# Performance work log

Hardware: AMD Instinct MI355X
Metric: run time of the kernel (lower is better)

Reference implementation:

```python
import jax, jax.numpy as jnp
import numpy as np
from math import sqrt

B, D, N, L, H, P = 32, 64, 254, 16, 128, 96  # batch, channels, patch_num, patch_len, hidden, pred_len


def positional_encoding(n, d):
    # standard sinusoidal PE, shape (n, d)
    pos = np.arange(n)[:, None].astype(np.float32)
    div = np.exp(np.arange(0, d, 2).astype(np.float32) * (-np.log(10000.0) / d))
    pe = np.zeros((n, d), dtype=np.float32)
    pe[:, 0::2] = np.sin(pos * div)
    pe[:, 1::2] = np.cos(pos * div)
    return jnp.asarray(pe)


def setup_inputs() -> dict:
    key = jax.random.key(0)
    ks = jax.random.split(key, 7)
    s = 0.05
    return {
        "x": jax.random.normal(ks[0], (B, D, N, L), dtype=jnp.float32),
        "W_enc": jax.random.normal(ks[1], (L, H), dtype=jnp.float32) * s,
        "b_enc": jax.random.normal(ks[2], (H,), dtype=jnp.float32) * s,
        "W1": jax.random.normal(ks[3], (L, H), dtype=jnp.float32) * s,
        "b1": jax.random.normal(ks[4], (H,), dtype=jnp.float32) * s,
        "W2": jax.random.normal(ks[5], (H, P), dtype=jnp.float32) * s,
        "b2": jax.random.normal(ks[6], (P,), dtype=jnp.float32) * s,
        "pos_embed": positional_encoding(N, H),  # buffer, not learned
    }


def reference(x, W_enc, b_enc, W1, b1, W2, b2, pos_embed):
    p = x  # detached clone in torch; same values
    # encode patches: (B,D,N,L) @ (L,H) -> (B,D,N,H), plus PE (N,H) broadcast
    c = jnp.einsum("bdnl,lh->bdnh", x, W_enc) + b_enc + pos_embed
    # score_i = sum_j c_i . c_j / sqrt(H)  ==  c_i . (sum_j c_j) / sqrt(H)
    csum = jnp.sum(c, axis=-2, keepdims=True)            # (B,D,1,H)
    score = jnp.sum(c * csum, axis=-1, keepdims=True) / sqrt(H)  # (B,D,N,1)
    weight = score / jnp.sum(jnp.abs(score), axis=-2, keepdims=True)
    pooled = jnp.sum(x * weight, axis=-2)                # (B,D,L)
    # FeedForward (dropout inactive at eval)
    h = jax.nn.leaky_relu(pooled @ W1 + b1, negative_slope=0.2)
    out = h @ W2 + b2                                    # (B,D,P)
    return out.transpose(0, 2, 1), p                     # (B,P,D), (B,D,N,L)
```

## Files before the change

### kernel.cpp

```cpp
#include <hip/hip_runtime.h>

#define B_ 32
#define D_ 64
#define N_ 254
#define L_ 16
#define H_ 128
#define P_ 96
#define PAIRS (B_*D_)
#define XPAIR (N_*L_)
#define OUT0  (B_*P_*D_)

#define WS_M    128
#define WS_VK   384
#define WS_BW   400
#define WS_BK   416
#define WS_G    432
#define WS_PK   4496
#define WS_KP   4752

typedef float f32x4 __attribute__((ext_vector_type(4)));

__global__ __launch_bounds__(256) void preK(const float* __restrict__ pos,
                                            float* __restrict__ ws) {
    __shared__ float red[256];
    int t = threadIdx.x;
    int h = t & 127, j = t >> 7;
    int n0 = blockIdx.x * 16;
    float acc = 0.f;
    #pragma unroll
    for (int r = 0; r < 8; r++) {
        int n = n0 + j + 2 * r;
        if (n < N_) acc += pos[n * H_ + h];
    }
    red[t] = acc;
    __syncthreads();
    if (t < 128) ws[WS_KP + blockIdx.x * 128 + t] = red[t] + red[t + 128];
}

__global__ __launch_bounds__(128) void pre2b(const float* __restrict__ W_enc,
                                             const float* __restrict__ b_enc,
                                             const float* __restrict__ pos,
                                             float* __restrict__ ws) {
    __shared__ float Ks[128], bL[128], pLDS[128], red[128], red2[128];
    __shared__ float WL[2048];
    int t = threadIdx.x;
    int n = blockIdx.x;

    {
        float b = b_enc[t];
        float s = 254.f * b;
        #pragma unroll
        for (int g = 0; g < 16; g++) s += ws[WS_KP + g * 128 + t];
        Ks[t] = s;
        bL[t] = b;
    }

    if (n < N_) {
        pLDS[t] = pos[n * H_ + t];
        __syncthreads();
        {
            int l = t >> 3, c = t & 7;
            const float* w = W_enc + l * H_ + c * 16;
            const float* p = pLDS + c * 16;
            float s = 0.f;
            #pragma unroll
            for (int i = 0; i < 16; i++) s += p[i] * w[i];
            red[t] = s;
            red2[t] = pLDS[t] * Ks[t];
        }
        __syncthreads();
        if (t < 16) {
            float s = 0.f;
            #pragma unroll
            for (int c = 0; c < 8; c++) s += red[t * 8 + c];
            ws[WS_G + n * 16 + t] = s;
        }
        if (t >= 64) {
            int lane = t - 64;
            float s = red2[lane] + red2[lane + 64];
            for (int off = 32; off; off >>= 1) s += __shfl_down(s, off);
            if (lane == 0) ws[WS_PK + n] = s;
        }
    } else {
        for (int i = t; i < 512; i += 128) {
            float4 v = ((const float4*)W_enc)[i];
            float* p = &WL[i * 4];
            p[0] = v.x; p[1] = v.y; p[2] = v.z; p[3] = v.w;
        }
        __syncthreads();
        #pragma unroll
        for (int e0 = 0; e0 < 2; e0++) {
            int e = e0 * 128 + t;
            int l1 = e >> 4, l2 = e & 15;
            float s = 0.f;
            for (int h = 0; h < H_; h++) s += WL[l1 * H_ + h] * WL[l2 * H_ + h];
            ws[WS_M + e] = s;
        }
        if (t < 16) {
            float s1 = 0.f, s2 = 0.f;
            for (int h = 0; h < H_; h++) {
                float w = WL[t * H_ + h];
                s1 += w * Ks[h];
                s2 += w * bL[h];
            }
            ws[WS_VK + t] = s1;
            ws[WS_BW + t] = s2;
        }
        if (t == 16) {
            float s = 0.f;
            for (int h = 0; h < H_; h++) s += bL[h] * Ks[h];
            ws[WS_BK] = s;
        }
    }
}

__global__ __launch_bounds__(256) void mainker(const float* __restrict__ x,
                                               const float* __restrict__ W1,
                                               const float* __restrict__ b1,
                                               const float* __restrict__ W2,
                                               const float* __restrict__ b2,
                                               const float* __restrict__ ws,
                                               float* __restrict__ out) {
    __shared__ float xf[N_ * 17 + 16];
    __shared__ float red[256];
    __shared__ float scoreS[N_];
    __shared__ float xsS[16], vS[16], pooledS[16], hS[128];
    __shared__ float s0S, denomS;

    int t  = threadIdx.x;
    int bd = blockIdx.x;

    const f32x4* xv = (const f32x4*)(x + (size_t)bd * XPAIR);
    f32x4*       cv = (f32x4*)(out + OUT0) + (size_t)bd * (XPAIR / 4);

    f32x4 v0 = xv[t];
    f32x4 v1 = xv[t + 256];
    f32x4 v2 = xv[t + 512];
    f32x4 v3 = {0.f, 0.f, 0.f, 0.f};
    bool has3 = (t < 248);
    if (has3) v3 = xv[t + 768];

    cv[t]       = v0;
    cv[t + 256] = v1;
    cv[t + 512] = v2;
    if (has3) cv[t + 768] = v3;

    #define UNPACK(vv, ii) { int idx = (ii) * 4; float* p = &xf[(idx >> 4) * 17 + (idx & 15)]; \
                             p[0] = vv[0]; p[1] = vv[1]; p[2] = vv[2]; p[3] = vv[3]; }
    UNPACK(v0, t); UNPACK(v1, t + 256); UNPACK(v2, t + 512);
    if (has3) UNPACK(v3, t + 768);
    #undef UNPACK
    __syncthreads();

    {
        int l = t & 15, g = t >> 4;
        float s = 0.f;
        for (int n = g; n < N_; n += 16) s += xf[n * 17 + l];
        red[t] = s;
    }
    __syncthreads();

    if (t < 16) {
        float xsv = 0.f;
        #pragma unroll
        for (int g = 0; g < 16; g++) xsv += red[g * 16 + t];
        xsS[t] = xsv;
        float s = ws[WS_VK + t];
        #pragma unroll
        for (int l2 = 0; l2 < 16; l2++) s += __shfl(xsv, l2) * ws[WS_M + l2 * 16 + t];
        vS[t] = s;
        float s0p = xsv * ws[WS_BW + t];
        #pragma unroll
        for (int off = 8; off; off >>= 1) s0p += __shfl_down(s0p, off);
        if (t == 0) s0S = ws[WS_BK] + s0p;
    }
    __syncthreads();

    if (t < N_) {
        const float* Gn = ws + WS_G + t * 16;
        float s = s0S + ws[WS_PK + t];
        #pragma unroll
        for (int l = 0; l < 16; l++) s += xf[t * 17 + l] * vS[l] + xsS[l] * Gn[l];
        scoreS[t] = s;
    }
    __syncthreads();

    if (t < 64) {
        float s = 0.f;
        for (int n = t; n < N_; n += 64) s += fabsf(scoreS[n]);
        for (int off = 32; off; off >>= 1) s += __shfl_down(s, off);
        if (t == 0) denomS = s;
    }
    {
        int l = t & 15, g = t >> 4;
        float s = 0.f;
        for (int n = g; n < N_; n += 16) s += xf[n * 17 + l] * scoreS[n];
        red[t] = s;
    }
    __syncthreads();
    if (t < 16) {
        float invd = 1.0f / denomS;
        float s = 0.f;
        #pragma unroll
        for (int g = 0; g < 16; g++) s += red[g * 16 + t];
        pooledS[t] = s * invd;
    }
    __syncthreads();

    if (t < 128) {
        float s = b1[t];
        #pragma unroll
        for (int l = 0; l < 16; l++) s += pooledS[l] * W1[l * H_ + t];
        hS[t] = s > 0.f ? s : 0.2f * s;
    }
    __syncthreads();

    if (t < 96) {
        float s = b2[t];
        for (int j = 0; j < 128; j++) s += hS[j] * W2[j * P_ + t];
        int b = bd >> 6, d = bd & 63;
        out[b * (P_ * D_) + t * D_ + d] = s;
    }
}

extern "C" void kernel_launch(void* const* d_in, const int* in_sizes, int n_in,
                              void* d_out, int out_size, void* d_ws, size_t ws_size,
                              hipStream_t stream) {
    const float* x     = (const float*)d_in[0];
    const float* W_enc = (const float*)d_in[1];
    const float* b_enc = (const float*)d_in[2];
    const float* W1    = (const float*)d_in[3];
    const float* b1    = (const float*)d_in[4];
    const float* W2    = (const float*)d_in[5];
    const float* b2    = (const float*)d_in[6];
    const float* pos   = (const float*)d_in[7];
    float* ws  = (float*)d_ws;
    float* out = (float*)d_out;

    hipLaunchKernelGGL(preK,   dim3(16),    dim3(256), 0, stream, pos, ws);
    hipLaunchKernelGGL(pre2b,  dim3(255),   dim3(128), 0, stream, W_enc, b_enc, pos, ws);
    hipLaunchKernelGGL(mainker, dim3(PAIRS), dim3(256), 0, stream, x, W1, b1, W2, b2, ws, out);
}
```

Measured before the change: 120.0 us.

## Keep x tile in registers instead of staging through padded LDS

Removes the padded shared-memory copy of each x tile and computes the column sums, scores and weighted pooling directly from the float4 registers each thread already loaded. The per-row score uses a 4-lane shuffle reduction, and the column reductions go through a float4 tree in LDS. This drops one full LDS write and several strided LDS read passes per block and shrinks LDS use, which may raise occupancy. The cost is extra shuffles and reduction barriers.

```diff
diff --git a/kernel.cpp b/kernel.cpp
--- a/kernel.cpp
+++ b/kernel.cpp
@@ -121,14 +121,14 @@
                                                const float* __restrict__ b2,
                                                const float* __restrict__ ws,
                                                float* __restrict__ out) {
-    __shared__ float xf[N_ * 17 + 16];
-    __shared__ float red[256];
-    __shared__ float scoreS[N_];
+    __shared__ f32x4 red4[256];
+    __shared__ float scoreS[256];
     __shared__ float xsS[16], vS[16], pooledS[16], hS[128];
     __shared__ float s0S, denomS;
 
     int t  = threadIdx.x;
     int bd = blockIdx.x;
+    int q  = t & 3, r0 = t >> 2;
 
     const f32x4* xv = (const f32x4*)(x + (size_t)bd * XPAIR);
     f32x4*       cv = (f32x4*)(out + OUT0) + (size_t)bd * (XPAIR / 4);
@@ -145,25 +145,15 @@
     cv[t + 512] = v2;
     if (has3) cv[t + 768] = v3;
 
-    #define UNPACK(vv, ii) { int idx = (ii) * 4; float* p = &xf[(idx >> 4) * 17 + (idx & 15)]; \
-                             p[0] = vv[0]; p[1] = vv[1]; p[2] = vv[2]; p[3] = vv[3]; }
-    UNPACK(v0, t); UNPACK(v1, t + 256); UNPACK(v2, t + 512);
-    if (has3) UNPACK(v3, t + 768);
-    #undef UNPACK
-    __syncthreads();
-
-    {
-        int l = t & 15, g = t >> 4;
-        float s = 0.f;
-        for (int n = g; n < N_; n += 16) s += xf[n * 17 + l];
-        red[t] = s;
-    }
+    red4[t] = v0 + v1 + v2 + v3;
+    __syncthreads();
+    if (t < 64) red4[t] = red4[t] + red4[t + 64] + red4[t + 128] + red4[t + 192];
     __syncthreads();
 
     if (t < 16) {
         float xsv = 0.f;
         #pragma unroll
-        for (int g = 0; g < 16; g++) xsv += red[g * 16 + t];
+        for (int m = 0; m < 16; m++) xsv += red4[m * 4 + (t >> 2)][t & 3];
         xsS[t] = xsv;
         float s = ws[WS_VK + t];
         #pragma unroll
@@ -176,12 +166,22 @@
     }
     __syncthreads();
 
-    if (t < N_) {
-        const float* Gn = ws + WS_G + t * 16;
-        float s = s0S + ws[WS_PK + t];
-        #pragma unroll
-        for (int l = 0; l < 16; l++) s += xf[t * 17 + l] * vS[l] + xsS[l] * Gn[l];
-        scoreS[t] = s;
+    {
+        float vq0 = vS[4*q], vq1 = vS[4*q+1], vq2 = vS[4*q+2], vq3 = vS[4*q+3];
+        float xq0 = xsS[4*q], xq1 = xsS[4*q+1], xq2 = xsS[4*q+2], xq3 = xsS[4*q+3];
+        #pragma unroll
+        for (int k = 0; k < 4; k++) {
+            if (k < 3 || has3) {
+                int rk = r0 + 64 * k;
+                f32x4 xk = (k == 0) ? v0 : (k == 1) ? v1 : (k == 2) ? v2 : v3;
+                f32x4 g  = *(const f32x4*)(ws + WS_G + rk * 16 + 4 * q);
+                float s = xk[0]*vq0 + xk[1]*vq1 + xk[2]*vq2 + xk[3]*vq3
+                        + xq0*g[0] + xq1*g[1] + xq2*g[2] + xq3*g[3];
+                s += __shfl_xor(s, 1);
+                s += __shfl_xor(s, 2);
+                if (q == 0) scoreS[rk] = s + s0S + ws[WS_PK + rk];
+            }
+        }
     }
     __syncthreads();
 
@@ -192,17 +192,18 @@
         if (t == 0) denomS = s;
     }
     {
-        int l = t & 15, g = t >> 4;
-        float s = 0.f;
-        for (int n = g; n < N_; n += 16) s += xf[n * 17 + l] * scoreS[n];
-        red[t] = s;
-    }
+        f32x4 p4 = v0 * scoreS[r0] + v1 * scoreS[r0 + 64] + v2 * scoreS[r0 + 128];
+        if (has3) p4 += v3 * scoreS[r0 + 192];
+        red4[t] = p4;
+    }
+    __syncthreads();
+    if (t < 64) red4[t] = red4[t] + red4[t + 64] + red4[t + 128] + red4[t + 192];
     __syncthreads();
     if (t < 16) {
         float invd = 1.0f / denomS;
         float s = 0.f;
         #pragma unroll
-        for (int g = 0; g < 16; g++) s += red[g * 16 + t];
+        for (int m = 0; m < 16; m++) s += red4[m * 4 + (t >> 2)][t & 3];
         pooledS[t] = s * invd;
     }
     __syncthreads();
```

After: 119.4 us, median of 2. About the same (-0.5%).
